# Optimization experiments

Hardware: AMD Instinct MI355X
Metric: run time of the kernel (lower is better)

## Reference

```python
import jax, jax.numpy as jnp
import numpy as np

# Architecture constants (from init_kwargs)
IN_DIM, D_MODEL, HEADDIM, D_STATE, EXPAND, OUT_DIM = 57, 64, 32, 32, 2, 6
D_INNER = EXPAND * D_MODEL          # 128
NHEADS = D_INNER // HEADDIM         # 4
D_CONV = 4                          # causal depthwise conv width (mamba default)
D_XBC = D_INNER + 2 * D_STATE       # 192 (x, B, C share the conv)
D_IN_PROJ = 2 * D_INNER + 2 * D_STATE + NHEADS  # z, xBC, dt -> 324
BATCH, SEQ = 16, 2048


def setup_inputs() -> dict:
    key = jax.random.key(0)
    ks = jax.random.split(key, 12)
    s = 0.02
    return {
        "x": jax.random.normal(ks[0], (BATCH, SEQ, IN_DIM), jnp.float32),
        "W_lin": jax.random.normal(ks[1], (IN_DIM, D_MODEL), jnp.float32) * s,
        "b_lin": jnp.zeros((D_MODEL,), jnp.float32),
        "W_in": jax.random.normal(ks[2], (D_MODEL, D_IN_PROJ), jnp.float32) * s,
        "conv_w": jax.random.normal(ks[3], (D_XBC, 1, D_CONV), jnp.float32) * 0.5,
        "conv_b": jnp.zeros((D_XBC,), jnp.float32),
        "dt_bias": jnp.log(jax.random.uniform(ks[4], (NHEADS,), jnp.float32, 0.001, 0.1)),
        "A_log": jnp.log(jnp.arange(1, NHEADS + 1, dtype=jnp.float32)),
        "D": jnp.ones((NHEADS,), jnp.float32),
        "norm_w": jnp.ones((D_INNER,), jnp.float32),
        "W_out": jax.random.normal(ks[5], (D_INNER, D_MODEL), jnp.float32) * s,
        "W_cls": jax.random.normal(ks[6], (D_MODEL, OUT_DIM), jnp.float32) * s,
        "b_cls": jnp.zeros((OUT_DIM,), jnp.float32),
    }


def _mamba_block(h, W_in, conv_w, conv_b, dt_bias, A_log, D, norm_w, W_out):
    B, L, _ = h.shape
    zxbcdt = h @ W_in                                   # [B,L,324]
    z = zxbcdt[..., :D_INNER]                           # gate [B,L,128]
    xBC = zxbcdt[..., D_INNER:D_INNER + D_XBC]          # [B,L,192]
    dt = zxbcdt[..., D_INNER + D_XBC:]                  # [B,L,H]

    # causal depthwise conv over time + silu
    xBC = jax.lax.conv_general_dilated(
        xBC.transpose(0, 2, 1), conv_w, (1,), [(D_CONV - 1, 0)],
        dimension_numbers=("NCH", "OIH", "NCH"), feature_group_count=D_XBC)
    xBC = jax.nn.silu(xBC + conv_b[None, :, None]).transpose(0, 2, 1)

    xs = xBC[..., :D_INNER].reshape(B, L, NHEADS, HEADDIM)   # [B,L,H,P]
    Bm = xBC[..., D_INNER:D_INNER + D_STATE]                 # [B,L,N]
    Cm = xBC[..., D_INNER + D_STATE:]                        # [B,L,N]

    dt = jax.nn.softplus(dt + dt_bias)                       # [B,L,H]
    A = -jnp.exp(A_log)                                      # [H]

    def step(hstate, t):
        dtt, xt, bt, ct = t                                  # [B,H],[B,H,P],[B,N],[B,N]
        decay = jnp.exp(dtt * A)[:, :, None, None]           # [B,H,1,1]
        hstate = hstate * decay + (dtt[:, :, None] * xt)[..., None] * bt[:, None, None, :]
        y = jnp.einsum("bhpn,bn->bhp", hstate, ct)
        return hstate, y

    h0 = jnp.zeros((B, NHEADS, HEADDIM, D_STATE), h.dtype)
    _, ys = jax.lax.scan(step, h0, (dt.transpose(1, 0, 2), xs.transpose(1, 0, 2, 3),
                                    Bm.transpose(1, 0, 2), Cm.transpose(1, 0, 2)))
    y = ys.transpose(1, 0, 2, 3) + D[None, None, :, None] * xs   # [B,L,H,P]
    y = y.reshape(B, L, D_INNER)

    # gated RMSNorm + out proj
    y = y * jax.nn.silu(z)
    y = y * jax.lax.rsqrt(jnp.mean(y * y, axis=-1, keepdims=True) + 1e-5) * norm_w
    return y @ W_out                                        # [B,L,D_MODEL]


def reference(x, W_lin, b_lin, W_in, conv_w, conv_b, dt_bias, A_log, D, norm_w,
              W_out, W_cls, b_cls):
    h = x @ W_lin + b_lin                                   # linear_in
    h = _mamba_block(h, W_in, conv_w, conv_b, dt_bias, A_log, D, norm_w, W_out)
    pooled = h.mean(axis=1)                                 # AdaptiveAvgPool1d(1)
    return pooled @ W_cls + b_cls                           # classifier [B,6]
```

## Files before the change

### kernel.cpp

```cpp
#include <hip/hip_runtime.h>
#include <hip/hip_fp16.h>
#include <cmath>

#define BATCH   16
#define SEQ     2048
#define IN_DIM  57
#define D_MODEL 64
#define HEADDIM 32
#define D_STATE 32
#define OUT_DIM 6
#define D_INNER 128
#define NHEADS  4
#define D_CONV  4
#define D_XBC   192
#define D_IN_PROJ 324
#define BL      (BATCH*SEQ)

#define NCHUNK  64
#define CLEN    (SEQ / NCHUNK)
#define SUBL    16
#define XDS     200

#define NT      21
#define WP_HALFS (NT * 2 * 64 * 8)

typedef _Float16 f16x8 __attribute__((ext_vector_type(8)));
typedef float    f32x4 __attribute__((ext_vector_type(4)));

#define OFF_WP   ((size_t)0)
#define OFF_BF   ((size_t)10752)
#define OFF_WOC  ((size_t)11088)
#define OFF_P    ((size_t)11856)
#define OFF_DC   ((size_t)15952)
#define OFF_ZB   ((size_t)147024)
#define OFF_CB   (OFF_ZB + (size_t)BL*64)
#define OFF_YB   (OFF_CB + (size_t)BL*16)
#define OFF_SB   (OFF_YB + (size_t)BL*64)

__global__ void fuse_w_kernel(const float* __restrict__ W_lin,
                              const float* __restrict__ b_lin,
                              const float* __restrict__ W_in,
                              const float* __restrict__ W_out,
                              const float* __restrict__ W_cls,
                              __half* __restrict__ Wph, float* __restrict__ bf,
                              float* __restrict__ Woc,
                              const float* __restrict__ b_cls,
                              float* __restrict__ out) {
    int idx = blockIdx.x * 256 + threadIdx.x;
    if (idx < 64 * 336) {
        int k = idx / 336;
        int n = idx - k * 336;
        float acc = 0.f;
        if (k < IN_DIM && n < D_IN_PROJ) {
#pragma unroll 8
            for (int m = 0; m < D_MODEL; ++m)
                acc += W_lin[k * D_MODEL + m] * W_in[m * D_IN_PROJ + n];
        }
        int t = n >> 4, nl = n & 15;
        int kb = k >> 5, kr = k & 31;
        size_t pidx = (((size_t)(t * 2 + kb) * 64) + (kr >> 3) * 16 + nl) * 8 + (kr & 7);
        Wph[pidx] = __float2half(acc);
    } else if (idx < 64 * 336 + D_IN_PROJ) {
        int n = idx - 64 * 336;
        float acc = 0.f;
#pragma unroll 8
        for (int m = 0; m < D_MODEL; ++m)
            acc += b_lin[m] * W_in[m * D_IN_PROJ + n];
        bf[n] = acc;
    } else if (idx < 64 * 336 + D_IN_PROJ + D_INNER * OUT_DIM) {
        int idx2 = idx - (64 * 336 + D_IN_PROJ);
        int i = idx2 / OUT_DIM;
        int o = idx2 - i * OUT_DIM;
        float acc = 0.f;
#pragma unroll 8
        for (int j = 0; j < D_MODEL; ++j)
            acc += W_out[i * D_MODEL + j] * W_cls[j * OUT_DIM + o];
        Woc[i * OUT_DIM + o] = acc;
    } else if (idx < 64 * 336 + D_IN_PROJ + D_INNER * OUT_DIM + BATCH * OUT_DIM) {
        int idx3 = idx - (64 * 336 + D_IN_PROJ + D_INNER * OUT_DIM);
        out[idx3] = b_cls[idx3 % OUT_DIM];
    }
}

__global__ __launch_bounds__(256) void mega1_kernel(
        const float* __restrict__ x,
        const __half* __restrict__ Wph, const float* __restrict__ bf,
        const float* __restrict__ conv_w, const float* __restrict__ conv_b,
        const float* __restrict__ dt_bias, const float* __restrict__ A_log,
        const float* __restrict__ Dp,
        __half* __restrict__ zbh,
        __half* __restrict__ sbuf, float* __restrict__ Pbuf,
        __half* __restrict__ ybuf, __half* __restrict__ Cbuf,
        float* __restrict__ Dcum) {
    __shared__ __align__(16) char smem[40112];
    __half* xsh        = (__half*)smem;
    __half (*zl)[128]  = (__half (*)[128])(smem + 6144);
    float (*xbt)[D_XBC]= (float (*)[D_XBC])smem;
    __half (*xdl)[XDS] = (__half (*)[XDS])(smem + 24576);
    __half (*yl)[D_INNER] = (__half (*)[D_INNER])(smem + 24576);
    float (*ddl)[8]    = (float (*)[8])(smem + 38576);
    float* dcl         = (float*)(smem + 39600);

    int b = blockIdx.x >> 6;
    int c = blockIdx.x & (NCHUNK - 1);
    int tid = threadIdx.x;
    long rbase = (long)b * SEQ + (long)c * CLEN;

    for (int i = tid; i < 48 * 64; i += 256) {
        int r = i >> 6, k = i & 63;
        float v = 0.f;
        if (r < 35 && k < IN_DIM && (c > 0 || r >= 3))
            v = x[(rbase - 3 + r) * IN_DIM + k];
        xsh[i ^ ((r & 7) << 3)] = __float2half(v);
    }
    __syncthreads();

    {
        int wid = tid >> 6, lane = tid & 63;
        int mrow = lane & 15, kg = lane >> 4;
        union { uint4 u; f16x8 f; } a[3][2];
#pragma unroll
        for (int mt = 0; mt < 3; ++mt)
#pragma unroll
            for (int kb = 0; kb < 2; ++kb) {
                int row = mt * 16 + mrow;
                int hidx = (row * 64 + kb * 32 + kg * 8) ^ ((row & 7) << 3);
                a[mt][kb].u = *(const uint4*)&xsh[hidx];
            }
        const uint4* wp4 = (const uint4*)Wph;
        for (int t = wid; t < NT; t += 4) {
            union { uint4 u; f16x8 f; } b0, b1;
            b0.u = wp4[(t * 2 + 0) * 64 + lane];
            b1.u = wp4[(t * 2 + 1) * 64 + lane];
            float bias = bf[t * 16 + mrow];
            f32x4 acc0 = {0.f, 0.f, 0.f, 0.f}, acc1 = acc0, acc2 = acc0;
            acc0 = __builtin_amdgcn_mfma_f32_16x16x32_f16(a[0][0].f, b0.f, acc0, 0, 0, 0);
            acc0 = __builtin_amdgcn_mfma_f32_16x16x32_f16(a[0][1].f, b1.f, acc0, 0, 0, 0);
            acc1 = __builtin_amdgcn_mfma_f32_16x16x32_f16(a[1][0].f, b0.f, acc1, 0, 0, 0);
            acc1 = __builtin_amdgcn_mfma_f32_16x16x32_f16(a[1][1].f, b1.f, acc1, 0, 0, 0);
            acc2 = __builtin_amdgcn_mfma_f32_16x16x32_f16(a[2][0].f, b0.f, acc2, 0, 0, 0);
            acc2 = __builtin_amdgcn_mfma_f32_16x16x32_f16(a[2][1].f, b1.f, acc2, 0, 0, 0);
            int n = t * 16 + mrow;
#pragma unroll
            for (int mt = 0; mt < 3; ++mt) {
                f32x4 av = (mt == 0) ? acc0 : (mt == 1) ? acc1 : acc2;
#pragma unroll
                for (int reg = 0; reg < 4; ++reg) {
                    int m = mt * 16 + kg * 4 + reg;
                    float v = av[reg] + bias;
                    if (t < 8) {
                        int zr = m - 3;
                        if (zr >= 0 && zr < 32) zl[zr][n] = __float2half(v);
                    } else {
                        int xc = n - 128;
                        if (m < 35 && xc < 196) xdl[m][xc] = __float2half(v);
                    }
                }
            }
        }
    }
    __syncthreads();

    {
        const uint4* zsrc = (const uint4*)&zl[0][0];
        uint4* zdst = (uint4*)(zbh + (size_t)rbase * D_INNER);
        zdst[tid]       = zsrc[tid];
        zdst[tid + 256] = zsrc[tid + 256];
    }
    __syncthreads();

    if (tid < D_XBC) {
        int ch = tid;
        float w0 = conv_w[ch*4+0], w1 = conv_w[ch*4+1];
        float w2 = conv_w[ch*4+2], w3 = conv_w[ch*4+3];
        float cb = conv_b[ch];
        float vm1 = 0.f, vm2 = 0.f, vm3 = 0.f;
        if (c > 0) {
            vm1 = __half2float(xdl[2][ch]);
            vm2 = __half2float(xdl[1][ch]);
            vm3 = __half2float(xdl[0][ch]);
        }
#pragma unroll
        for (int i = 0; i < CLEN; ++i) {
            float v0 = __half2float(xdl[i + 3][ch]);
            float a = cb + v0 * w3 + vm1 * w2 + vm2 * w1 + vm3 * w0;
            xbt[i][ch] = a / (1.f + expf(-a));
            vm3 = vm2; vm2 = vm1; vm1 = v0;
        }
    } else {
        int idx = tid - D_XBC;
        int h = idx >> 4;
        int i0 = idx & 15;
        float db = dt_bias[h];
        float nA = -expf(A_log[h]);
#pragma unroll
        for (int i = i0; i < CLEN; i += 16) {
            float v = __half2float(xdl[i + 3][192 + h]) + db;
            float dtv = (v > 20.f) ? v : log1pf(expf(v));
            ddl[i][h * 2]     = dtv;
            ddl[i][h * 2 + 1] = expf(dtv * nA);
        }
    }
    __syncthreads();

    int h = tid >> 6, lane = tid & 63;
    int p = lane >> 1, n0 = (lane & 1) * 16;
    float Dh = Dp[h];
    float4 s0 = make_float4(0.f,0.f,0.f,0.f), s1 = s0, s2 = s0, s3 = s0;
    float pacc = 1.f;
#pragma unroll 4
    for (int i = 0; i < CLEN; ++i) {
        float dtv = ddl[i][h * 2];
        float dec = ddl[i][h * 2 + 1];
        float xv = xbt[i][h * HEADDIM + p];
        const float* Bp = &xbt[i][D_INNER + n0];
        const float* Cp = &xbt[i][D_INNER + D_STATE + n0];
        float4 B0 = *(const float4*)(Bp + 0);
        float4 B1 = *(const float4*)(Bp + 4);
        float4 B2 = *(const float4*)(Bp + 8);
        float4 B3 = *(const float4*)(Bp + 12);
        float4 C0 = *(const float4*)(Cp + 0);
        float4 C1 = *(const float4*)(Cp + 4);
        float4 C2 = *(const float4*)(Cp + 8);
        float4 C3 = *(const float4*)(Cp + 12);
        float coef = dtv * xv;
        s0.x = s0.x*dec + coef*B0.x; s0.y = s0.y*dec + coef*B0.y;
        s0.z = s0.z*dec + coef*B0.z; s0.w = s0.w*dec + coef*B0.w;
        s1.x = s1.x*dec + coef*B1.x; s1.y = s1.y*dec + coef*B1.y;
        s1.z = s1.z*dec + coef*B1.z; s1.w = s1.w*dec + coef*B1.w;
        s2.x = s2.x*dec + coef*B2.x; s2.y = s2.y*dec + coef*B2.y;
        s2.z = s2.z*dec + coef*B2.z; s2.w = s2.w*dec + coef*B2.w;
        s3.x = s3.x*dec + coef*B3.x; s3.y = s3.y*dec + coef*B3.y;
        s3.z = s3.z*dec + coef*B3.z; s3.w = s3.w*dec + coef*B3.w;
        pacc *= dec;
        float part = s0.x*C0.x + s0.y*C0.y + s0.z*C0.z + s0.w*C0.w
                   + s1.x*C1.x + s1.y*C1.y + s1.z*C1.z + s1.w*C1.w
                   + s2.x*C2.x + s2.y*C2.y + s2.z*C2.z + s2.w*C2.w
                   + s3.x*C3.x + s3.y*C3.y + s3.z*C3.z + s3.w*C3.w;
        part += __shfl_xor(part, 1);
        if (lane == 0) dcl[i * 4 + h] = pacc;
        if ((lane & 1) == 0)
            yl[i][h * HEADDIM + p] = __float2half(part + Dh * xv);
    }
    int bh = b * NHEADS + h;
    __half2 hs[8];
    hs[0] = __floats2half2_rn(s0.x, s0.y); hs[1] = __floats2half2_rn(s0.z, s0.w);
    hs[2] = __floats2half2_rn(s1.x, s1.y); hs[3] = __floats2half2_rn(s1.z, s1.w);
    hs[4] = __floats2half2_rn(s2.x, s2.y); hs[5] = __floats2half2_rn(s2.z, s2.w);
    hs[6] = __floats2half2_rn(s3.x, s3.y); hs[7] = __floats2half2_rn(s3.z, s3.w);
    uint4* sp = (uint4*)(sbuf + ((size_t)bh * NCHUNK + c) * 1024) + lane * 2;
    sp[0] = *(uint4*)&hs[0];
    sp[1] = *(uint4*)&hs[4];
    if (lane == 0) Pbuf[bh * NCHUNK + c] = pacc;
    __syncthreads();
    {
        const uint4* ysrc = (const uint4*)&yl[0][0];
        uint4* ydst = (uint4*)(ybuf + (size_t)rbase * D_INNER);
        ydst[tid]       = ysrc[tid];
        ydst[tid + 256] = ysrc[tid + 256];
    }
    for (int idx = tid; idx < CLEN * 16; idx += 256) {
        int r  = idx >> 4;
        int n2 = (idx & 15) * 2;
        __half2 hv = __floats2half2_rn(xbt[r][D_INNER + D_STATE + n2],
                                       xbt[r][D_INNER + D_STATE + n2 + 1]);
        *((__half2*)(Cbuf + ((size_t)rbase + r) * D_STATE + n2)) = hv;
    }
    if (tid < CLEN * 4) Dcum[(size_t)rbase * 4 + tid] = dcl[tid];
}

__global__ __launch_bounds__(256) void scan_phase2_kernel(
        __half* __restrict__ sbuf, const float* __restrict__ Pbuf) {
    __shared__ unsigned sl[NCHUNK][128];
    __shared__ float Pl[NCHUNK];
    int bh = blockIdx.x >> 2;
    int q  = blockIdx.x & 3;
    int tid = threadIdx.x;
    unsigned* s32 = (unsigned*)sbuf;
    size_t base = (size_t)bh * NCHUNK * 512 + (size_t)q * 128;
    if (tid < NCHUNK) Pl[tid] = Pbuf[bh * NCHUNK + tid];
    for (int k = tid; k < NCHUNK * 128; k += 256) {
        int c = k >> 7, j = k & 127;
        sl[c][j] = s32[base + (size_t)c * 512 + j];
    }
    __syncthreads();
    if (tid < 128) {
        float rx = 0.f, ry = 0.f;
        unsigned v = sl[0][tid];
#pragma unroll 8
        for (int c = 0; c < NCHUNK; ++c) {
            unsigned vn = (c + 1 < NCHUNK) ? sl[c + 1][tid] : 0u;
            float Pv = Pl[c];
            __half2 hv = *(__half2*)&v;
            float2 t = __half22float2(hv);
            __half2 hr = __floats2half2_rn(rx, ry);
            sl[c][tid] = *(unsigned*)&hr;
            rx = rx * Pv + t.x;
            ry = ry * Pv + t.y;
            v = vn;
        }
    }
    __syncthreads();
    for (int k = tid; k < NCHUNK * 128; k += 256) {
        int c = k >> 7, j = k & 127;
        s32[base + (size_t)c * 512 + j] = sl[c][j];
    }
}

__global__ __launch_bounds__(256) void scan_phase3_kernel(
        const __half* __restrict__ ybuf, const __half* __restrict__ Cbuf,
        const float* __restrict__ Dcum, const __half* __restrict__ zbh,
        const __half* __restrict__ sbuf, const float* __restrict__ norm_w,
        const float* __restrict__ Woc, float* __restrict__ out) {
    int b  = blockIdx.x >> 7;
    int sc = blockIdx.x & 127;
    int c  = sc >> 1;
    int tid = threadIdx.x;
    __shared__ float ylds[SUBL][D_INNER];
    __shared__ float dcl[SUBL * 4];
    __shared__ float red[4][D_INNER];
    __shared__ float snw[D_INNER];
    size_t rbase = (size_t)b * SEQ + (size_t)sc * SUBL;
    int h = tid >> 6, lane = tid & 63;
    int p = lane >> 1, n0 = (lane & 1) * 16;
    int bh = b * NHEADS + h;
    const uint4* sp = (const uint4*)(sbuf + ((size_t)bh * NCHUNK + c) * 1024) + lane * 2;
    uint4 u0 = sp[0], u1 = sp[1];
    {
        const __half2* ysrc = (const __half2*)(ybuf + rbase * D_INNER);
#pragma unroll
        for (int k = 0; k < 4; ++k) {
            int idx = tid + k * 256;
            float2 f = __half22float2(ysrc[idx]);
            int r  = idx >> 6;
            int c2 = (idx & 63) * 2;
            ylds[r][c2]     = f.x;
            ylds[r][c2 + 1] = f.y;
        }
    }
    if (tid < SUBL * 4) dcl[tid] = Dcum[rbase * 4 + tid];
    float4 s0, s1, s2, s3;
    {
        const __half2* hp0 = (const __half2*)&u0;
        const __half2* hp1 = (const __half2*)&u1;
        float2 f;
        f = __half22float2(hp0[0]); s0.x = f.x; s0.y = f.y;
        f = __half22float2(hp0[1]); s0.z = f.x; s0.w = f.y;
        f = __half22float2(hp0[2]); s1.x = f.x; s1.y = f.y;
        f = __half22float2(hp0[3]); s1.z = f.x; s1.w = f.y;
        f = __half22float2(hp1[0]); s2.x = f.x; s2.y = f.y;
        f = __half22float2(hp1[1]); s2.z = f.x; s2.w = f.y;
        f = __half22float2(hp1[2]); s3.x = f.x; s3.y = f.y;
        f = __half22float2(hp1[3]); s3.z = f.x; s3.w = f.y;
    }
    __syncthreads();
#pragma unroll 4
    for (int i = 0; i < SUBL; ++i) {
        const uint4* cp = (const uint4*)(Cbuf + (rbase + i) * D_STATE + n0);
        uint4 ca = cp[0], cb = cp[1];
        const __half2* cha = (const __half2*)&ca;
        const __half2* chb = (const __half2*)&cb;
        float2 f0 = __half22float2(cha[0]);
        float2 f1 = __half22float2(cha[1]);
        float2 f2 = __half22float2(cha[2]);
        float2 f3 = __half22float2(cha[3]);
        float2 f4 = __half22float2(chb[0]);
        float2 f5 = __half22float2(chb[1]);
        float2 f6 = __half22float2(chb[2]);
        float2 f7 = __half22float2(chb[3]);
        float part = s0.x*f0.x + s0.y*f0.y + s0.z*f1.x + s0.w*f1.y
                   + s1.x*f2.x + s1.y*f2.y + s1.z*f3.x + s1.w*f3.y
                   + s2.x*f4.x + s2.y*f4.y + s2.z*f5.x + s2.w*f5.y
                   + s3.x*f6.x + s3.y*f6.y + s3.z*f7.x + s3.w*f7.y;
        part += __shfl_xor(part, 1);
        if ((lane & 1) == 0)
            ylds[i][h * HEADDIM + p] += dcl[i * 4 + h] * part;
    }
    __syncthreads();
    float acc0 = 0.f, acc1 = 0.f;
    for (int r = h; r < SUBL; r += 4) {
        size_t bl = rbase + r;
        float2 yv = *(const float2*)(&ylds[r][lane * 2]);
        float2 zv = __half22float2(*((const __half2*)(zbh + bl * D_INNER) + lane));
        float g0 = yv.x * (zv.x / (1.f + expf(-zv.x)));
        float g1 = yv.y * (zv.y / (1.f + expf(-zv.y)));
        float sq = g0 * g0 + g1 * g1;
#pragma unroll
        for (int m = 1; m < 64; m <<= 1) sq += __shfl_xor(sq, m);
        float rms = 1.0f / sqrtf(sq * (1.f / 128.f) + 1e-5f);
        acc0 += g0 * rms;
        acc1 += g1 * rms;
    }
    red[h][lane * 2]     = acc0;
    red[h][lane * 2 + 1] = acc1;
    __syncthreads();
    if (tid < D_INNER)
        snw[tid] = (red[0][tid] + red[1][tid] + red[2][tid] + red[3][tid])
                   * norm_w[tid];
    __syncthreads();
    if (tid < OUT_DIM) {
        float acc = 0.f;
#pragma unroll 8
        for (int i = 0; i < D_INNER; ++i)
            acc += snw[i] * Woc[i * OUT_DIM + tid];
        atomicAdd(&out[b * OUT_DIM + tid], acc * (1.f / (float)SEQ));
    }
}

extern "C" void kernel_launch(void* const* d_in, const int* in_sizes, int n_in,
                              void* d_out, int out_size, void* d_ws, size_t ws_size,
                              hipStream_t stream) {
    const float* x       = (const float*)d_in[0];
    const float* W_lin   = (const float*)d_in[1];
    const float* b_lin   = (const float*)d_in[2];
    const float* W_in    = (const float*)d_in[3];
    const float* conv_w  = (const float*)d_in[4];
    const float* conv_b  = (const float*)d_in[5];
    const float* dt_bias = (const float*)d_in[6];
    const float* A_log   = (const float*)d_in[7];
    const float* Dp      = (const float*)d_in[8];
    const float* norm_w  = (const float*)d_in[9];
    const float* W_out   = (const float*)d_in[10];
    const float* W_cls   = (const float*)d_in[11];
    const float* b_cls   = (const float*)d_in[12];
    float* out = (float*)d_out;

    float* ws = (float*)d_ws;
    __half* Wph  = (__half*)(ws + OFF_WP);
    float* bf    = ws + OFF_BF;
    float* Woc   = ws + OFF_WOC;
    float* Pbuf  = ws + OFF_P;
    float* Dcum  = ws + OFF_DC;
    __half* zbh  = (__half*)(ws + OFF_ZB);
    __half* Cbh  = (__half*)(ws + OFF_CB);
    __half* ybh  = (__half*)(ws + OFF_YB);
    __half* sbuf = (__half*)(ws + OFF_SB);

    int nfw = 64 * 336 + D_IN_PROJ + D_INNER * OUT_DIM + BATCH * OUT_DIM;
    fuse_w_kernel<<<(nfw + 255) / 256, 256, 0, stream>>>(
        W_lin, b_lin, W_in, W_out, W_cls, Wph, bf, Woc, b_cls, out);

    mega1_kernel<<<BATCH * NCHUNK, 256, 0, stream>>>(
        x, Wph, bf, conv_w, conv_b, dt_bias, A_log, Dp,
        zbh, sbuf, Pbuf, ybh, Cbh, Dcum);

    scan_phase2_kernel<<<256, 256, 0, stream>>>(sbuf, Pbuf);

    scan_phase3_kernel<<<BATCH * 128, 256, 0, stream>>>(
        ybh, Cbh, Dcum, zbh, sbuf, norm_w, Woc, out);
}
```

Baseline: 150.4 us.

## Replace sequential intra-chunk scan with MFMA-based chunked SSD matmuls

Replaces the per-timestep recurrent scan inside each 32-step chunk with the chunked state-space-duality formulation. It computes C·Bᵀ, applies a causal decay mask built from prefix-summed log-decays, and multiplies by x, plus a weighted xᵀB matmul for the chunk-end state, all using fp16 16x16x32 MFMA instructions. Conv outputs are now stored as fp16 in swizzled shared-memory tiles, and the y buffer is written in the MFMA fragment layout, so the downstream kernel's load indexing is changed to match. The goal is to swap a serial FMA chain for matrix-core throughput, at the cost of extra fp16 rounding in the intermediate products and more complex layouts.

New measurement: 144.1 us. 1.04x faster.

```diff
diff --git a/kernel.cpp b/kernel.cpp
--- a/kernel.cpp
+++ b/kernel.cpp
@@ -22,10 +22,23 @@
 #define XDS     200
 
 #define NT      21
-#define WP_HALFS (NT * 2 * 64 * 8)
 
 typedef _Float16 f16x8 __attribute__((ext_vector_type(8)));
 typedef float    f32x4 __attribute__((ext_vector_type(4)));
+
+#define OXT   0
+#define OB16  8192
+#define OBT   10240
+#define OC16  12288
+#define OXDL  14336
+#define OML   14336
+#define OSL   14336
+#define OYP   22528
+#define ODTL  30720
+#define OLSL  31232
+#define OWL2  31744
+#define ODCL  32000
+#define SMEM_SZ 32512
 
 #define OFF_WP   ((size_t)0)
 #define OFF_BF   ((size_t)10752)
@@ -36,6 +49,13 @@
 #define OFF_CB   (OFF_ZB + (size_t)BL*64)
 #define OFF_YB   (OFF_CB + (size_t)BL*16)
 #define OFF_SB   (OFF_YB + (size_t)BL*64)
+
+__device__ __forceinline__ int swz(int row, int j) {
+    return row * 64 + (((j >> 3) ^ (row & 3)) << 4) + ((j & 7) << 1);
+}
+__device__ __forceinline__ int swz4(int row, int kg) {
+    return row * 64 + ((kg ^ (row & 3)) << 4);
+}
 
 __global__ void fuse_w_kernel(const float* __restrict__ W_lin,
                               const float* __restrict__ b_lin,
@@ -92,14 +112,10 @@
         __half* __restrict__ sbuf, float* __restrict__ Pbuf,
         __half* __restrict__ ybuf, __half* __restrict__ Cbuf,
         float* __restrict__ Dcum) {
-    __shared__ __align__(16) char smem[40112];
+    __shared__ __align__(16) char smem[SMEM_SZ];
     __half* xsh        = (__half*)smem;
     __half (*zl)[128]  = (__half (*)[128])(smem + 6144);
-    float (*xbt)[D_XBC]= (float (*)[D_XBC])smem;
-    __half (*xdl)[XDS] = (__half (*)[XDS])(smem + 24576);
-    __half (*yl)[D_INNER] = (__half (*)[D_INNER])(smem + 24576);
-    float (*ddl)[8]    = (float (*)[8])(smem + 38576);
-    float* dcl         = (float*)(smem + 39600);
+    __half (*xdl)[XDS] = (__half (*)[XDS])(smem + OXDL);
 
     int b = blockIdx.x >> 6;
     int c = blockIdx.x & (NCHUNK - 1);
@@ -169,8 +185,28 @@
     }
     __syncthreads();
 
-    if (tid < D_XBC) {
-        int ch = tid;
+    if (tid < D_INNER) {
+        int p = tid;
+        float w0 = conv_w[p*4+0], w1 = conv_w[p*4+1];
+        float w2 = conv_w[p*4+2], w3 = conv_w[p*4+3];
+        float cb = conv_b[p];
+        float vm1 = 0.f, vm2 = 0.f, vm3 = 0.f;
+        if (c > 0) {
+            vm1 = __half2float(xdl[2][p]);
+            vm2 = __half2float(xdl[1][p]);
+            vm3 = __half2float(xdl[0][p]);
+        }
+#pragma unroll
+        for (int i = 0; i < CLEN; ++i) {
+            float v0 = __half2float(xdl[i + 3][p]);
+            float a = cb + v0 * w3 + vm1 * w2 + vm2 * w1 + vm3 * w0;
+            float sv = a / (1.f + expf(-a));
+            *(__half*)(smem + OXT + swz(p, i)) = __float2half(sv);
+            vm3 = vm2; vm2 = vm1; vm1 = v0;
+        }
+    } else if (tid < D_INNER + D_STATE) {
+        int n = tid - D_INNER;
+        int ch = D_INNER + n;
         float w0 = conv_w[ch*4+0], w1 = conv_w[ch*4+1];
         float w2 = conv_w[ch*4+2], w3 = conv_w[ch*4+3];
         float cb = conv_b[ch];
@@ -184,7 +220,28 @@
         for (int i = 0; i < CLEN; ++i) {
             float v0 = __half2float(xdl[i + 3][ch]);
             float a = cb + v0 * w3 + vm1 * w2 + vm2 * w1 + vm3 * w0;
-            xbt[i][ch] = a / (1.f + expf(-a));
+            __half hv = __float2half(a / (1.f + expf(-a)));
+            *(__half*)(smem + OB16 + swz(i, n)) = hv;
+            *(__half*)(smem + OBT  + swz(n, i)) = hv;
+            vm3 = vm2; vm2 = vm1; vm1 = v0;
+        }
+    } else if (tid < D_XBC) {
+        int n = tid - (D_INNER + D_STATE);
+        int ch = D_INNER + D_STATE + n;
+        float w0 = conv_w[ch*4+0], w1 = conv_w[ch*4+1];
+        float w2 = conv_w[ch*4+2], w3 = conv_w[ch*4+3];
+        float cb = conv_b[ch];
+        float vm1 = 0.f, vm2 = 0.f, vm3 = 0.f;
+        if (c > 0) {
+            vm1 = __half2float(xdl[2][ch]);
+            vm2 = __half2float(xdl[1][ch]);
+            vm3 = __half2float(xdl[0][ch]);
+        }
+#pragma unroll
+        for (int i = 0; i < CLEN; ++i) {
+            float v0 = __half2float(xdl[i + 3][ch]);
+            float a = cb + v0 * w3 + vm1 * w2 + vm2 * w1 + vm3 * w0;
+            *(__half*)(smem + OC16 + swz(i, n)) = __float2half(a / (1.f + expf(-a)));
             vm3 = vm2; vm2 = vm1; vm1 = v0;
         }
     } else {
@@ -192,81 +249,164 @@
         int h = idx >> 4;
         int i0 = idx & 15;
         float db = dt_bias[h];
-        float nA = -expf(A_log[h]);
+        float* dtl = (float*)(smem + ODTL);
 #pragma unroll
         for (int i = i0; i < CLEN; i += 16) {
             float v = __half2float(xdl[i + 3][192 + h]) + db;
-            float dtv = (v > 20.f) ? v : log1pf(expf(v));
-            ddl[i][h * 2]     = dtv;
-            ddl[i][h * 2 + 1] = expf(dtv * nA);
-        }
-    }
-    __syncthreads();
-
-    int h = tid >> 6, lane = tid & 63;
-    int p = lane >> 1, n0 = (lane & 1) * 16;
+            dtl[h * 32 + i] = (v > 20.f) ? v : log1pf(expf(v));
+        }
+    }
+    __syncthreads();
+
+    int h = tid >> 6, l = tid & 63;
+    int col = l & 15, kg = l >> 4;
+    int li = l & 31;
+    float nA = -expf(A_log[h]);
     float Dh = Dp[h];
-    float4 s0 = make_float4(0.f,0.f,0.f,0.f), s1 = s0, s2 = s0, s3 = s0;
-    float pacc = 1.f;
-#pragma unroll 4
-    for (int i = 0; i < CLEN; ++i) {
-        float dtv = ddl[i][h * 2];
-        float dec = ddl[i][h * 2 + 1];
-        float xv = xbt[i][h * HEADDIM + p];
-        const float* Bp = &xbt[i][D_INNER + n0];
-        const float* Cp = &xbt[i][D_INNER + D_STATE + n0];
-        float4 B0 = *(const float4*)(Bp + 0);
-        float4 B1 = *(const float4*)(Bp + 4);
-        float4 B2 = *(const float4*)(Bp + 8);
-        float4 B3 = *(const float4*)(Bp + 12);
-        float4 C0 = *(const float4*)(Cp + 0);
-        float4 C1 = *(const float4*)(Cp + 4);
-        float4 C2 = *(const float4*)(Cp + 8);
-        float4 C3 = *(const float4*)(Cp + 12);
-        float coef = dtv * xv;
-        s0.x = s0.x*dec + coef*B0.x; s0.y = s0.y*dec + coef*B0.y;
-        s0.z = s0.z*dec + coef*B0.z; s0.w = s0.w*dec + coef*B0.w;
-        s1.x = s1.x*dec + coef*B1.x; s1.y = s1.y*dec + coef*B1.y;
-        s1.z = s1.z*dec + coef*B1.z; s1.w = s1.w*dec + coef*B1.w;
-        s2.x = s2.x*dec + coef*B2.x; s2.y = s2.y*dec + coef*B2.y;
-        s2.z = s2.z*dec + coef*B2.z; s2.w = s2.w*dec + coef*B2.w;
-        s3.x = s3.x*dec + coef*B3.x; s3.y = s3.y*dec + coef*B3.y;
-        s3.z = s3.z*dec + coef*B3.z; s3.w = s3.w*dec + coef*B3.w;
-        pacc *= dec;
-        float part = s0.x*C0.x + s0.y*C0.y + s0.z*C0.z + s0.w*C0.w
-                   + s1.x*C1.x + s1.y*C1.y + s1.z*C1.z + s1.w*C1.w
-                   + s2.x*C2.x + s2.y*C2.y + s2.z*C2.z + s2.w*C2.w
-                   + s3.x*C3.x + s3.y*C3.y + s3.z*C3.z + s3.w*C3.w;
-        part += __shfl_xor(part, 1);
-        if (lane == 0) dcl[i * 4 + h] = pacc;
-        if ((lane & 1) == 0)
-            yl[i][h * HEADDIM + p] = __float2half(part + Dh * xv);
-    }
-    int bh = b * NHEADS + h;
-    __half2 hs[8];
-    hs[0] = __floats2half2_rn(s0.x, s0.y); hs[1] = __floats2half2_rn(s0.z, s0.w);
-    hs[2] = __floats2half2_rn(s1.x, s1.y); hs[3] = __floats2half2_rn(s1.z, s1.w);
-    hs[4] = __floats2half2_rn(s2.x, s2.y); hs[5] = __floats2half2_rn(s2.z, s2.w);
-    hs[6] = __floats2half2_rn(s3.x, s3.y); hs[7] = __floats2half2_rn(s3.z, s3.w);
-    uint4* sp = (uint4*)(sbuf + ((size_t)bh * NCHUNK + c) * 1024) + lane * 2;
-    sp[0] = *(uint4*)&hs[0];
-    sp[1] = *(uint4*)&hs[4];
-    if (lane == 0) Pbuf[bh * NCHUNK + c] = pacc;
-    __syncthreads();
-    {
-        const uint4* ysrc = (const uint4*)&yl[0][0];
-        uint4* ydst = (uint4*)(ybuf + (size_t)rbase * D_INNER);
-        ydst[tid]       = ysrc[tid];
-        ydst[tid + 256] = ysrc[tid + 256];
-    }
-    for (int idx = tid; idx < CLEN * 16; idx += 256) {
-        int r  = idx >> 4;
-        int n2 = (idx & 15) * 2;
-        __half2 hv = __floats2half2_rn(xbt[r][D_INNER + D_STATE + n2],
-                                       xbt[r][D_INNER + D_STATE + n2 + 1]);
-        *((__half2*)(Cbuf + ((size_t)rbase + r) * D_STATE + n2)) = hv;
-    }
-    if (tid < CLEN * 4) Dcum[(size_t)rbase * 4 + tid] = dcl[tid];
+    float* dtl = (float*)(smem + ODTL);
+    float* lsl = (float*)(smem + OLSL);
+    float* dcl = (float*)(smem + ODCL);
+    __half2* wl2 = (__half2*)(smem + OWL2);
+
+    {
+        float dtv = dtl[h * 32 + li];
+        float ls = dtv * nA;
+#pragma unroll
+        for (int d = 1; d < 32; d <<= 1) {
+            float t = __shfl_up(ls, d, 32);
+            if (li >= d) ls += t;
+        }
+        float cd = expf(ls);
+        float lsE = __shfl(ls, 31, 32);
+        float w = expf(lsE - ls) * dtv;
+        float wn = __shfl_down(w, 1, 32);
+        if (l < 32) {
+            lsl[h * 32 + li] = ls;
+            dcl[li * 4 + h] = cd;
+            if ((li & 1) == 0) wl2[h * 16 + (li >> 1)] = __floats2half2_rn(w, wn);
+            if (li == 31) Pbuf[(b * NHEADS + h) * NCHUNK + c] = cd;
+        }
+    }
+
+    f32x4 g[2][2];
+    {
+        union { uint4 u; f16x8 f; } ac[2], bb[2];
+#pragma unroll
+        for (int mt = 0; mt < 2; ++mt)
+            ac[mt].u = *(const uint4*)(smem + OC16 + swz4(mt * 16 + col, kg));
+#pragma unroll
+        for (int nt = 0; nt < 2; ++nt)
+            bb[nt].u = *(const uint4*)(smem + OB16 + swz4(nt * 16 + col, kg));
+#pragma unroll
+        for (int mt = 0; mt < 2; ++mt)
+#pragma unroll
+            for (int nt = 0; nt < 2; ++nt) {
+                f32x4 z = {0.f, 0.f, 0.f, 0.f};
+                g[mt][nt] = __builtin_amdgcn_mfma_f32_16x16x32_f16(ac[mt].f, bb[nt].f, z, 0, 0, 0);
+            }
+    }
+
+    {
+        const float* lslh = lsl + h * 32;
+        const float* dtlh = dtl + h * 32;
+#pragma unroll
+        for (int nt = 0; nt < 2; ++nt) {
+            int j = nt * 16 + col;
+            float lsj = lslh[j], dtj = dtlh[j];
+#pragma unroll
+            for (int mt = 0; mt < 2; ++mt)
+#pragma unroll
+                for (int r = 0; r < 4; ++r) {
+                    int i = mt * 16 + kg * 4 + r;
+                    float mv = 0.f;
+                    if (j < i)       mv = g[mt][nt][r] * expf(lslh[i] - lsj) * dtj;
+                    else if (j == i) mv = g[mt][nt][r] * dtj + Dh;
+                    *(__half*)(smem + OML + h * 2048 + swz(i, j)) = __float2half(mv);
+                }
+        }
+    }
+
+    {
+        union { uint4 u; f16x8 f; } am[2], bx[2];
+#pragma unroll
+        for (int mt = 0; mt < 2; ++mt)
+            am[mt].u = *(const uint4*)(smem + OML + h * 2048 + swz4(mt * 16 + col, kg));
+#pragma unroll
+        for (int nt = 0; nt < 2; ++nt)
+            bx[nt].u = *(const uint4*)(smem + OXT + swz4(h * 32 + nt * 16 + col, kg));
+        f32x4 y[2][2];
+#pragma unroll
+        for (int mt = 0; mt < 2; ++mt)
+#pragma unroll
+            for (int nt = 0; nt < 2; ++nt) {
+                f32x4 z = {0.f, 0.f, 0.f, 0.f};
+                y[mt][nt] = __builtin_amdgcn_mfma_f32_16x16x32_f16(am[mt].f, bx[nt].f, z, 0, 0, 0);
+            }
+#pragma unroll
+        for (int mt = 0; mt < 2; ++mt) {
+            __half2 hp[4];
+            hp[0] = __floats2half2_rn(y[mt][0][0], y[mt][0][1]);
+            hp[1] = __floats2half2_rn(y[mt][0][2], y[mt][0][3]);
+            hp[2] = __floats2half2_rn(y[mt][1][0], y[mt][1][1]);
+            hp[3] = __floats2half2_rn(y[mt][1][2], y[mt][1][3]);
+            *(uint4*)(smem + OYP + mt * 4096 + (h * 64 + l) * 16) = *(uint4*)hp;
+        }
+    }
+
+    {
+        union { uint4 u; __half2 p[4]; f16x8 f; } aw[2], bt[2];
+#pragma unroll
+        for (int mt = 0; mt < 2; ++mt) {
+            aw[mt].u = *(const uint4*)(smem + OXT + swz4(h * 32 + mt * 16 + col, kg));
+            const __half2* wp = wl2 + h * 16 + kg * 4;
+#pragma unroll
+            for (int t = 0; t < 4; ++t) aw[mt].p[t] = __hmul2(aw[mt].p[t], wp[t]);
+        }
+#pragma unroll
+        for (int nt = 0; nt < 2; ++nt)
+            bt[nt].u = *(const uint4*)(smem + OBT + swz4(nt * 16 + col, kg));
+        f32x4 s[2][2];
+#pragma unroll
+        for (int mt = 0; mt < 2; ++mt)
+#pragma unroll
+            for (int nt = 0; nt < 2; ++nt) {
+                f32x4 z = {0.f, 0.f, 0.f, 0.f};
+                s[mt][nt] = __builtin_amdgcn_mfma_f32_16x16x32_f16(aw[mt].f, bt[nt].f, z, 0, 0, 0);
+            }
+#pragma unroll
+        for (int mt = 0; mt < 2; ++mt)
+#pragma unroll
+            for (int nt = 0; nt < 2; ++nt)
+#pragma unroll
+                for (int r = 0; r < 4; ++r) {
+                    int p = mt * 16 + kg * 4 + r;
+                    int n = nt * 16 + col;
+                    *(__half*)(smem + OSL + h * 2048 + p * 64 + n * 2) =
+                        __float2half(s[mt][nt][r]);
+                }
+    }
+    __syncthreads();
+
+#pragma unroll
+    for (int k2 = 0; k2 < 2; ++k2) {
+        int idx = tid + k2 * 256;
+        int hh = idx >> 7, off = idx & 127;
+        *(uint4*)(sbuf + (((size_t)(b * NHEADS + hh) * NCHUNK + c) << 10) + off * 8) =
+            *(uint4*)(smem + OSL + hh * 2048 + off * 16);
+    }
+#pragma unroll
+    for (int k2 = 0; k2 < 2; ++k2) {
+        int idx = tid + k2 * 256;
+        int mt = idx >> 8, off = idx & 255;
+        *(uint4*)(ybuf + (size_t)rbase * D_INNER + mt * 2048 + off * 8) =
+            *(uint4*)(smem + OYP + mt * 4096 + off * 16);
+    }
+    if (tid < 128) {
+        int i = tid >> 2, blk = tid & 3;
+        *(uint4*)(Cbuf + ((size_t)rbase + i) * D_STATE + blk * 8) =
+            *(uint4*)(smem + OC16 + i * 64 + ((blk ^ (i & 3)) << 4));
+    }
+    if (tid < 128) Dcum[(size_t)rbase * 4 + tid] = dcl[tid];
 }
 
 __global__ __launch_bounds__(256) void scan_phase2_kernel(
@@ -327,15 +467,22 @@
     const uint4* sp = (const uint4*)(sbuf + ((size_t)bh * NCHUNK + c) * 1024) + lane * 2;
     uint4 u0 = sp[0], u1 = sp[1];
     {
-        const __half2* ysrc = (const __half2*)(ybuf + rbase * D_INNER);
+        const __half2* ysrc = (const __half2*)(
+            ybuf + ((size_t)b * SEQ + (size_t)c * CLEN) * D_INNER + (size_t)(sc & 1) * 2048);
 #pragma unroll
         for (int k = 0; k < 4; ++k) {
             int idx = tid + k * 256;
             float2 f = __half22float2(ysrc[idx]);
-            int r  = idx >> 6;
-            int c2 = (idx & 63) * 2;
-            ylds[r][c2]     = f.x;
-            ylds[r][c2 + 1] = f.y;
+            int pos = idx * 2;
+            int hh = pos >> 9;
+            int rem = pos & 511;
+            int fl = rem >> 3;
+            int rr = rem & 7;
+            int nt = rr >> 2, r0 = rr & 3;
+            int row = ((fl >> 4) << 2) + r0;
+            int colc = hh * 32 + nt * 16 + (fl & 15);
+            ylds[row][colc]     = f.x;
+            ylds[row + 1][colc] = f.y;
         }
     }
     if (tid < SUBL * 4) dcl[tid] = Dcum[rbase * 4 + tid];
```
